# Kernel optimization log

Measured on AMD Instinct MI355X. Metric: run time of the kernel, lower is better.

Reference implementation:

```python
import jax, jax.numpy as jnp
import numpy as np
import math

B, S, H = 512, 100, 1024
A, N = 128, 8
TAU = 1.0


def make_pe(seq_len, hidden):
    # PositionalEncoding buffer: pe[s, 0::2]=sin(pos*div), pe[s,1::2]=cos(pos*div)
    pos = jnp.arange(seq_len, dtype=jnp.float32)[:, None]          # [S,1]
    div = jnp.exp(jnp.arange(0, hidden, 2, dtype=jnp.float32) * (-math.log(10000.0) / hidden))
    pe = jnp.zeros((seq_len, hidden), dtype=jnp.float32)
    pe = pe.at[:, 0::2].set(jnp.sin(pos * div))
    pe = pe.at[:, 1::2].set(jnp.cos(pos * div))
    return pe                                                      # [S,H]


def setup_inputs() -> dict:
    key = jax.random.key(0)
    kx, kq, kk, kg = jax.random.split(key, 4)
    x = jax.random.normal(kx, (B, S, H), dtype=jnp.float32)
    # torch Linear weight layout: [out_features, in_features]
    Wq = jax.random.normal(kq, (A * N, H), dtype=jnp.float32) * (1.0 / math.sqrt(H))
    Wk = jax.random.normal(kk, (A * N, H), dtype=jnp.float32) * (1.0 / math.sqrt(H))
    # pre-sampled standard Gumbel noise (deterministic reference)
    u = jax.random.uniform(kg, (B * N, S), dtype=jnp.float32, minval=1e-6, maxval=1.0 - 1e-6)
    gumbel = -jnp.log(-jnp.log(u))
    return {"x": x, "Wq": Wq, "Wk": Wk, "gumbel": gumbel}


def reference(x, Wq, Wk, gumbel):
    b, s, h = x.shape
    pos_emb = x + make_pe(s, h)[None]                              # [B,S,H]
    Q = (pos_emb @ Wq.T).reshape(b, s, N, A).transpose(0, 2, 1, 3)  # [B,N,S,A]
    K = (pos_emb @ Wk.T).reshape(b, s, N, A).transpose(0, 2, 1, 3)  # [B,N,S,A]
    # original: sum_t (Q . K_t) / sqrt(H) / S  ==  Q . (sum_t K_t) / (sqrt(H)*S)
    Ksum = K.sum(axis=2)                                           # [B,N,A]
    logits = jnp.einsum('bnsa,bna->bns', Q, Ksum) / (math.sqrt(h) * s)
    y = (logits.reshape(b * N, s) + gumbel) / TAU
    soft = jax.nn.softmax(y, axis=-1)
    hard = jax.nn.one_hot(jnp.argmax(y, axis=-1), s, dtype=soft.dtype)
    # straight-through (forward value == hard one-hot)
    alphas = (hard - jax.lax.stop_gradient(soft) + soft).reshape(b, N, s)
    out = jnp.einsum('bns,bsh->bnh', alphas, x)                    # gather selected timesteps
    return out
```

## Files before the change

kernel.cpp:

```cpp
#include <hip/hip_runtime.h>
#include <float.h>
#include <math.h>

#define Bc 512
#define Sc 100
#define Hc 1024
#define Ac 128
#define Nc 8
#define AS_ST 68
#define BS_ST 132

__global__ __launch_bounds__(256) void pe_kernel(float* __restrict__ pe){
  int s = blockIdx.x;
  int t = threadIdx.x;
  const float fac = (float)(-9.210340371976184 / 1024.0);
  for(int i = t; i < Hc/2; i += 256){
    float div = expf((float)(2*i) * fac);
    float a = (float)s * div;
    pe[s*Hc + 2*i]     = sinf(a);
    pe[s*Hc + 2*i + 1] = cosf(a);
  }
}

__global__ __launch_bounds__(256) void pesum_kernel(const float* __restrict__ pe, float* __restrict__ pesum){
  int h = blockIdx.x*256 + threadIdx.x;
  float acc = 0.f;
  for(int s = 0; s < Sc; ++s) acc += pe[s*Hc + h];
  pesum[h] = acc;
}

__global__ __launch_bounds__(256) void xsum_kernel(const float* __restrict__ x, const float* __restrict__ pesum,
                                                   float* __restrict__ xsp){
  int b = blockIdx.x;
  int q = blockIdx.y;
  int t = threadIdx.x;
  const float4* xr = (const float4*)(x + (size_t)b*Sc*Hc);
  float4 acc;
  if(q == 0) acc = ((const float4*)pesum)[t];
  else       acc = make_float4(0.f,0.f,0.f,0.f);
  int s0 = q*25;
  #pragma unroll 5
  for(int s = s0; s < s0+25; ++s){
    float4 v = xr[s*(Hc/4) + t];
    acc.x += v.x; acc.y += v.y; acc.z += v.z; acc.w += v.w;
  }
  ((float4*)(xsp + ((size_t)b*4 + q)*Hc))[t] = acc;
}

__global__ __launch_bounds__(256) void xsred_kernel(const float* __restrict__ xsp, float* __restrict__ xs){
  int b = blockIdx.x, t = threadIdx.x;
  const float4* p = (const float4*)(xsp + (size_t)b*4*Hc);
  float4 a = p[t], b1 = p[256+t], c = p[512+t], d = p[768+t];
  a.x += b1.x + c.x + d.x;
  a.y += b1.y + c.y + d.y;
  a.z += b1.z + c.z + d.z;
  a.w += b1.w + c.w + d.w;
  ((float4*)(xs + (size_t)b*Hc))[t] = a;
}

__global__ __launch_bounds__(256) void ksum_gemm2(const float* __restrict__ xs, const float* __restrict__ Wk,
                                                  float* __restrict__ Ksum4){
  __shared__ float As[32*AS_ST];
  __shared__ float Bs[32*BS_ST];
  const int t = threadIdx.x;
  const int j0 = blockIdx.x*128, b0 = blockIdx.y*64, ks = blockIdx.z;
  const int ty = t>>4, tx = t&15;
  float acc[4][8];
  #pragma unroll
  for(int i = 0; i < 4; ++i)
    #pragma unroll
    for(int j = 0; j < 8; ++j) acc[i][j] = 0.f;

  const int mA = (t>>3) & 63;
  for(int k0 = ks*256; k0 < ks*256 + 256; k0 += 32){
    float4 af[2], bf[4];
    #pragma unroll
    for(int i = 0; i < 2; ++i){
      int id = t + i*256; int m = id>>3, q = id&7;
      af[i] = *(const float4*)(xs + ((size_t)(b0+m)<<10) + k0 + q*4);
    }
    #pragma unroll
    for(int i = 0; i < 4; ++i){
      int id = t + i*256; int r = id>>3, c = id&7;
      bf[i] = *(const float4*)(Wk + ((size_t)(j0+r)<<10) + k0 + c*4);
    }
    __syncthreads();
    #pragma unroll
    for(int i = 0; i < 2; ++i){
      int id = t + i*256; int m = id>>3, q = id&7;
      As[(q*4+0)*AS_ST + m] = af[i].x;
      As[(q*4+1)*AS_ST + m] = af[i].y;
      As[(q*4+2)*AS_ST + m] = af[i].z;
      As[(q*4+3)*AS_ST + m] = af[i].w;
    }
    #pragma unroll
    for(int i = 0; i < 4; ++i){
      int id = t + i*256; int r = id>>3, c = id&7;
      Bs[(c*4+0)*BS_ST + r] = bf[i].x;
      Bs[(c*4+1)*BS_ST + r] = bf[i].y;
      Bs[(c*4+2)*BS_ST + r] = bf[i].z;
      Bs[(c*4+3)*BS_ST + r] = bf[i].w;
    }
    __syncthreads();
    #pragma unroll 8
    for(int kk = 0; kk < 32; ++kk){
      float4 a4 = *(const float4*)&As[kk*AS_ST + ty*4];
      float4 bu = *(const float4*)&Bs[kk*BS_ST + tx*4];
      float4 bv = *(const float4*)&Bs[kk*BS_ST + 64 + tx*4];
      float a[4] = {a4.x, a4.y, a4.z, a4.w};
      float bb[8] = {bu.x,bu.y,bu.z,bu.w, bv.x,bv.y,bv.z,bv.w};
      #pragma unroll
      for(int i = 0; i < 4; ++i)
        #pragma unroll
        for(int j = 0; j < 8; ++j)
          acc[i][j] = fmaf(a[i], bb[j], acc[i][j]);
    }
  }
  (void)mA;
  #pragma unroll
  for(int i = 0; i < 4; ++i){
    float* cp = Ksum4 + (((size_t)ks*Bc + b0 + ty*4 + i)<<10) + j0 + tx*4;
    *(float4*)cp        = make_float4(acc[i][0],acc[i][1],acc[i][2],acc[i][3]);
    *(float4*)(cp + 64) = make_float4(acc[i][4],acc[i][5],acc[i][6],acc[i][7]);
  }
}

__global__ __launch_bounds__(256) void ksred_kernel(const float* __restrict__ Ksum4, float* __restrict__ Ksum){
  int b = blockIdx.x, t = threadIdx.x;
  const float4* p = (const float4*)(Ksum4 + ((size_t)b<<10));
  const size_t sl = (size_t)Bc*Hc/4;
  float4 a = p[t], b1 = p[sl+t], c = p[2*sl+t], d = p[3*sl+t];
  a.x += b1.x + c.x + d.x;
  a.y += b1.y + c.y + d.y;
  a.z += b1.z + c.z + d.z;
  a.w += b1.w + c.w + d.w;
  ((float4*)(Ksum + ((size_t)b<<10)))[t] = a;
}

__global__ __launch_bounds__(256) void v_gemm2(const float* __restrict__ Ksum, const float* __restrict__ Wq,
                                               float* __restrict__ v){
  __shared__ float As[32*AS_ST];
  __shared__ float Bs[32*BS_ST];
  const int t = threadIdx.x;
  const int h0 = blockIdx.x*128, b0 = blockIdx.y*64, n = blockIdx.z;
  const int ty = t>>4, tx = t&15;
  float acc[4][8];
  #pragma unroll
  for(int i = 0; i < 4; ++i)
    #pragma unroll
    for(int j = 0; j < 8; ++j) acc[i][j] = 0.f;

  for(int k0 = 0; k0 < Ac; k0 += 32){
    float4 af[2], bf[4];
    #pragma unroll
    for(int i = 0; i < 2; ++i){
      int id = t + i*256; int m = id>>3, q = id&7;
      af[i] = *(const float4*)(Ksum + ((size_t)(b0+m)<<10) + n*Ac + k0 + q*4);
    }
    #pragma unroll
    for(int i = 0; i < 4; ++i){
      int id = t + i*256; int kk = id>>5, q = id&31;
      bf[i] = *(const float4*)(Wq + ((size_t)(n*Ac + k0 + kk)<<10) + h0 + q*4);
    }
    __syncthreads();
    #pragma unroll
    for(int i = 0; i < 2; ++i){
      int id = t + i*256; int m = id>>3, q = id&7;
      As[(q*4+0)*AS_ST + m] = af[i].x;
      As[(q*4+1)*AS_ST + m] = af[i].y;
      As[(q*4+2)*AS_ST + m] = af[i].z;
      As[(q*4+3)*AS_ST + m] = af[i].w;
    }
    #pragma unroll
    for(int i = 0; i < 4; ++i){
      int id = t + i*256; int kk = id>>5, q = id&31;
      *(float4*)&Bs[kk*BS_ST + q*4] = bf[i];
    }
    __syncthreads();
    #pragma unroll 8
    for(int kk = 0; kk < 32; ++kk){
      float4 a4 = *(const float4*)&As[kk*AS_ST + ty*4];
      float4 bu = *(const float4*)&Bs[kk*BS_ST + tx*4];
      float4 bv = *(const float4*)&Bs[kk*BS_ST + 64 + tx*4];
      float a[4] = {a4.x, a4.y, a4.z, a4.w};
      float bb[8] = {bu.x,bu.y,bu.z,bu.w, bv.x,bv.y,bv.z,bv.w};
      #pragma unroll
      for(int i = 0; i < 4; ++i)
        #pragma unroll
        for(int j = 0; j < 8; ++j)
          acc[i][j] = fmaf(a[i], bb[j], acc[i][j]);
    }
  }
  #pragma unroll
  for(int i = 0; i < 4; ++i){
    float* cp = v + (((size_t)(b0 + ty*4 + i)*Nc + n)<<10) + h0 + tx*4;
    *(float4*)cp        = make_float4(acc[i][0],acc[i][1],acc[i][2],acc[i][3]);
    *(float4*)(cp + 64) = make_float4(acc[i][4],acc[i][5],acc[i][6],acc[i][7]);
  }
}

__global__ __launch_bounds__(1024) void attn_kernel(const float* __restrict__ x, const float* __restrict__ pe,
                                                    const float* __restrict__ v, const float* __restrict__ g,
                                                    float* __restrict__ out){
  __shared__ float4 tile[1600];
  __shared__ float part[8][Nc][104];
  __shared__ int sidx[Nc];
  const int b = blockIdx.x;
  const int t = threadIdx.x;
  const int lane = t & 63;
  const int w  = __builtin_amdgcn_readfirstlane(t >> 6);
  const int kq = w & 7, sh = w >> 3;

  const int r1 = t >> 4, c1 = t & 15;
  const bool has2 = (t < 576);
  const int e2 = t + 1024;
  const int r2 = e2 >> 4, c2 = e2 & 15;

  const float* xb = x + (size_t)b*Sc*Hc;
  const float* vb = v + (size_t)b*Nc*Hc;

  int rw = sh*64 + lane;
  int r  = (rw < Sc) ? rw : (Sc-1);
  const bool valid = (rw < Sc);

  float acc[Nc];
  #pragma unroll
  for(int n = 0; n < Nc; ++n) acc[n] = 0.f;

  float4 xv1 = *(const float4*)(xb + r1*Hc + c1*4);
  float4 pv1 = *(const float4*)(pe + r1*Hc + c1*4);
  float4 xv2 = make_float4(0,0,0,0), pv2 = make_float4(0,0,0,0);
  if(has2){ xv2 = *(const float4*)(xb + r2*Hc + c2*4);
            pv2 = *(const float4*)(pe + r2*Hc + c2*4); }

  for(int kt = 0; kt < 16; ++kt){
    __syncthreads();
    tile[r1*16 + (c1 ^ (r1&7))] = make_float4(xv1.x+pv1.x, xv1.y+pv1.y, xv1.z+pv1.z, xv1.w+pv1.w);
    if(has2)
      tile[r2*16 + (c2 ^ (r2&7))] = make_float4(xv2.x+pv2.x, xv2.y+pv2.y, xv2.z+pv2.z, xv2.w+pv2.w);
    if(kt < 15){
      int ko = (kt+1)*64;
      xv1 = *(const float4*)(xb + r1*Hc + ko + c1*4);
      pv1 = *(const float4*)(pe + r1*Hc + ko + c1*4);
      if(has2){ xv2 = *(const float4*)(xb + r2*Hc + ko + c2*4);
                pv2 = *(const float4*)(pe + r2*Hc + ko + c2*4); }
    }
    __syncthreads();
    #pragma unroll
    for(int j = 0; j < 2; ++j){
      float4 xe = tile[r*16 + ((kq*2 + j) ^ (r&7))];
      const float* vk = vb + kt*64 + kq*8 + j*4;
      #pragma unroll
      for(int n = 0; n < Nc; ++n){
        const float* vn = vk + n*Hc;
        acc[n] = fmaf(xe.x, vn[0], acc[n]);
        acc[n] = fmaf(xe.y, vn[1], acc[n]);
        acc[n] = fmaf(xe.z, vn[2], acc[n]);
        acc[n] = fmaf(xe.w, vn[3], acc[n]);
      }
    }
  }
  if(valid){
    #pragma unroll
    for(int n = 0; n < Nc; ++n) part[kq][n][rw] = acc[n];
  }
  __syncthreads();

  if(w < Nc){
    int n = w, j = lane;
    float best = -FLT_MAX; int bidx = 0;
    #pragma unroll
    for(int i = 0; i < 2; ++i){
      int s2 = j + 64*i;
      if(s2 < Sc){
        float dot = 0.f;
        #pragma unroll
        for(int q = 0; q < 8; ++q) dot += part[q][n][s2];
        float y = dot/3200.0f + g[(size_t)(b*Nc + n)*Sc + s2];
        if(y > best){ best = y; bidx = s2; }
      }
    }
    #pragma unroll
    for(int m = 32; m >= 1; m >>= 1){
      float ob = __shfl_xor(best, m, 64);
      int   oi = __shfl_xor(bidx, m, 64);
      if(ob > best || (ob == best && oi < bidx)){ best = ob; bidx = oi; }
    }
    if(j == 0) sidx[n] = bidx;
  }
  __syncthreads();

  const float4* xb4 = (const float4*)xb;
  float4* ob4 = (float4*)(out + (size_t)b*Nc*Hc);
  #pragma unroll
  for(int i = 0; i < 2; ++i){
    int idx = i*1024 + t;
    int nn = idx >> 8, c = idx & 255;
    ob4[idx] = xb4[sidx[nn]*256 + c];
  }
}

extern "C" void kernel_launch(void* const* d_in, const int* in_sizes, int n_in,
                              void* d_out, int out_size, void* d_ws, size_t ws_size,
                              hipStream_t stream) {
  const float* x  = (const float*)d_in[0];
  const float* Wq = (const float*)d_in[1];
  const float* Wk = (const float*)d_in[2];
  const float* g  = (const float*)d_in[3];
  float* out = (float*)d_out;

  char* ws = (char*)d_ws;
  float* pe    = (float*)(ws);
  float* pesum = (float*)(ws +    409600);
  float* xsp   = (float*)(ws +    413696);
  float* Ksum4 = (float*)(ws +    413696);
  float* xs    = (float*)(ws +   8802304);
  float* Ksum  = (float*)(ws +  10899456);
  float* v     = (float*)(ws +  12996608);

  pe_kernel   <<<100, 256, 0, stream>>>(pe);
  pesum_kernel<<<4,   256, 0, stream>>>(pe, pesum);
  xsum_kernel <<<dim3(512,4), 256, 0, stream>>>(x, pesum, xsp);
  xsred_kernel<<<512, 256, 0, stream>>>(xsp, xs);
  ksum_gemm2  <<<dim3(8,8,4), 256, 0, stream>>>(xs, Wk, Ksum4);
  ksred_kernel<<<512, 256, 0, stream>>>(Ksum4, Ksum);
  v_gemm2     <<<dim3(8,8,8), 256, 0, stream>>>(Ksum, Wq, v);
  attn_kernel <<<512, 1024, 0, stream>>>(x, pe, v, g, out);
}
```

Baseline: 146.4 us.

## Restructure attention logits kernel: wave-per-row with register-resident v and shuffle reductions

```diff
diff --git a/kernel.cpp b/kernel.cpp
--- a/kernel.cpp
+++ b/kernel.cpp
@@ -71,7 +71,6 @@
     #pragma unroll
     for(int j = 0; j < 8; ++j) acc[i][j] = 0.f;
 
-  const int mA = (t>>3) & 63;
   for(int k0 = ks*256; k0 < ks*256 + 256; k0 += 32){
     float4 af[2], bf[4];
     #pragma unroll
@@ -116,7 +115,6 @@
           acc[i][j] = fmaf(a[i], bb[j], acc[i][j]);
     }
   }
-  (void)mA;
   #pragma unroll
   for(int i = 0; i < 4; ++i){
     float* cp = Ksum4 + (((size_t)ks*Bc + b0 + ty*4 + i)<<10) + j0 + tx*4;
@@ -199,70 +197,61 @@
   }
 }
 
-__global__ __launch_bounds__(1024) void attn_kernel(const float* __restrict__ x, const float* __restrict__ pe,
-                                                    const float* __restrict__ v, const float* __restrict__ g,
-                                                    float* __restrict__ out){
-  __shared__ float4 tile[1600];
-  __shared__ float part[8][Nc][104];
+__global__ __launch_bounds__(1024, 8) void attn_kernel(const float* __restrict__ x, const float* __restrict__ pe,
+                                                       const float* __restrict__ v, const float* __restrict__ g,
+                                                       float* __restrict__ out){
+  __shared__ float lg[Sc][9];
   __shared__ int sidx[Nc];
   const int b = blockIdx.x;
   const int t = threadIdx.x;
   const int lane = t & 63;
-  const int w  = __builtin_amdgcn_readfirstlane(t >> 6);
-  const int kq = w & 7, sh = w >> 3;
-
-  const int r1 = t >> 4, c1 = t & 15;
-  const bool has2 = (t < 576);
-  const int e2 = t + 1024;
-  const int r2 = e2 >> 4, c2 = e2 & 15;
-
-  const float* xb = x + (size_t)b*Sc*Hc;
-  const float* vb = v + (size_t)b*Nc*Hc;
-
-  int rw = sh*64 + lane;
-  int r  = (rw < Sc) ? rw : (Sc-1);
-  const bool valid = (rw < Sc);
-
-  float acc[Nc];
-  #pragma unroll
-  for(int n = 0; n < Nc; ++n) acc[n] = 0.f;
-
-  float4 xv1 = *(const float4*)(xb + r1*Hc + c1*4);
-  float4 pv1 = *(const float4*)(pe + r1*Hc + c1*4);
-  float4 xv2 = make_float4(0,0,0,0), pv2 = make_float4(0,0,0,0);
-  if(has2){ xv2 = *(const float4*)(xb + r2*Hc + c2*4);
-            pv2 = *(const float4*)(pe + r2*Hc + c2*4); }
-
-  for(int kt = 0; kt < 16; ++kt){
-    __syncthreads();
-    tile[r1*16 + (c1 ^ (r1&7))] = make_float4(xv1.x+pv1.x, xv1.y+pv1.y, xv1.z+pv1.z, xv1.w+pv1.w);
-    if(has2)
-      tile[r2*16 + (c2 ^ (r2&7))] = make_float4(xv2.x+pv2.x, xv2.y+pv2.y, xv2.z+pv2.z, xv2.w+pv2.w);
-    if(kt < 15){
-      int ko = (kt+1)*64;
-      xv1 = *(const float4*)(xb + r1*Hc + ko + c1*4);
-      pv1 = *(const float4*)(pe + r1*Hc + ko + c1*4);
-      if(has2){ xv2 = *(const float4*)(xb + r2*Hc + ko + c2*4);
-                pv2 = *(const float4*)(pe + r2*Hc + ko + c2*4); }
-    }
-    __syncthreads();
-    #pragma unroll
-    for(int j = 0; j < 2; ++j){
-      float4 xe = tile[r*16 + ((kq*2 + j) ^ (r&7))];
-      const float* vk = vb + kt*64 + kq*8 + j*4;
+  const int w = t >> 6;
+
+  const float4* vb4 = (const float4*)(v + (size_t)b*Nc*Hc);
+  float4 vr[Nc][4];
+  #pragma unroll
+  for(int n = 0; n < Nc; ++n)
+    #pragma unroll
+    for(int i = 0; i < 4; ++i)
+      vr[n][i] = vb4[n*256 + i*64 + lane];
+
+  const float4* xb4 = (const float4*)(x + (size_t)b*Sc*Hc);
+  const float4* pe4 = (const float4*)pe;
+
+  for(int s = w; s < Sc; s += 16){
+    float4 e[4];
+    #pragma unroll
+    for(int i = 0; i < 4; ++i){
+      float4 xv = xb4[s*256 + i*64 + lane];
+      float4 pv = pe4[s*256 + i*64 + lane];
+      e[i] = make_float4(xv.x+pv.x, xv.y+pv.y, xv.z+pv.z, xv.w+pv.w);
+    }
+    float acc[Nc];
+    #pragma unroll
+    for(int n = 0; n < Nc; ++n){
+      float a = 0.f;
       #pragma unroll
-      for(int n = 0; n < Nc; ++n){
-        const float* vn = vk + n*Hc;
-        acc[n] = fmaf(xe.x, vn[0], acc[n]);
-        acc[n] = fmaf(xe.y, vn[1], acc[n]);
-        acc[n] = fmaf(xe.z, vn[2], acc[n]);
-        acc[n] = fmaf(xe.w, vn[3], acc[n]);
+      for(int i = 0; i < 4; ++i){
+        a = fmaf(e[i].x, vr[n][i].x, a);
+        a = fmaf(e[i].y, vr[n][i].y, a);
+        a = fmaf(e[i].z, vr[n][i].z, a);
+        a = fmaf(e[i].w, vr[n][i].w, a);
       }
-    }
-  }
-  if(valid){
-    #pragma unroll
-    for(int n = 0; n < Nc; ++n) part[kq][n][rw] = acc[n];
+      acc[n] = a;
+    }
+    #pragma unroll
+    for(int m = 1; m <= 4; m <<= 1)
+      #pragma unroll
+      for(int n = 0; n < Nc; ++n)
+        acc[n] += __shfl_xor(acc[n], m, 64);
+    float keep = acc[0];
+    #pragma unroll
+    for(int n = 1; n < Nc; ++n)
+      keep = ((lane & 7) == n) ? acc[n] : keep;
+    #pragma unroll
+    for(int m = 8; m <= 32; m <<= 1)
+      keep += __shfl_xor(keep, m, 64);
+    if(lane < Nc) lg[s][lane] = keep;
   }
   __syncthreads();
 
@@ -273,10 +262,7 @@
     for(int i = 0; i < 2; ++i){
       int s2 = j + 64*i;
       if(s2 < Sc){
-        float dot = 0.f;
-        #pragma unroll
-        for(int q = 0; q < 8; ++q) dot += part[q][n][s2];
-        float y = dot/3200.0f + g[(size_t)(b*Nc + n)*Sc + s2];
+        float y = lg[s2][n]/3200.0f + g[(size_t)(b*Nc + n)*Sc + s2];
         if(y > best){ best = y; bidx = s2; }
       }
     }
@@ -290,7 +276,6 @@
   }
   __syncthreads();
 
-  const float4* xb4 = (const float4*)xb;
   float4* ob4 = (float4*)(out + (size_t)b*Nc*Hc);
   #pragma unroll
   for(int i = 0; i < 2; ++i){
```

After: 408.6 us. +179.1%, slower.

## Prefetch next K-chunk into registers in GEMMs and raise ksum split-K to 8

Applied to the files above, without the earlier changes.

```diff
diff --git a/kernel.cpp b/kernel.cpp
--- a/kernel.cpp
+++ b/kernel.cpp
@@ -59,7 +59,7 @@
 }
 
 __global__ __launch_bounds__(256) void ksum_gemm2(const float* __restrict__ xs, const float* __restrict__ Wk,
-                                                  float* __restrict__ Ksum4){
+                                                  float* __restrict__ Ksum8){
   __shared__ float As[32*AS_ST];
   __shared__ float Bs[32*BS_ST];
   const int t = threadIdx.x;
@@ -71,19 +71,20 @@
     #pragma unroll
     for(int j = 0; j < 8; ++j) acc[i][j] = 0.f;
 
-  const int mA = (t>>3) & 63;
-  for(int k0 = ks*256; k0 < ks*256 + 256; k0 += 32){
-    float4 af[2], bf[4];
-    #pragma unroll
-    for(int i = 0; i < 2; ++i){
-      int id = t + i*256; int m = id>>3, q = id&7;
-      af[i] = *(const float4*)(xs + ((size_t)(b0+m)<<10) + k0 + q*4);
-    }
-    #pragma unroll
-    for(int i = 0; i < 4; ++i){
-      int id = t + i*256; int r = id>>3, c = id&7;
-      bf[i] = *(const float4*)(Wk + ((size_t)(j0+r)<<10) + k0 + c*4);
-    }
+  const int kb = ks*128;
+  float4 af[2], bf[4], afn[2], bfn[4];
+  #pragma unroll
+  for(int i = 0; i < 2; ++i){
+    int id = t + i*256; int m = id>>3, q = id&7;
+    af[i] = *(const float4*)(xs + ((size_t)(b0+m)<<10) + kb + q*4);
+  }
+  #pragma unroll
+  for(int i = 0; i < 4; ++i){
+    int id = t + i*256; int r = id>>3, c = id&7;
+    bf[i] = *(const float4*)(Wk + ((size_t)(j0+r)<<10) + kb + c*4);
+  }
+
+  for(int c0 = 0; c0 < 4; ++c0){
     __syncthreads();
     #pragma unroll
     for(int i = 0; i < 2; ++i){
@@ -100,6 +101,19 @@
       Bs[(c*4+1)*BS_ST + r] = bf[i].y;
       Bs[(c*4+2)*BS_ST + r] = bf[i].z;
       Bs[(c*4+3)*BS_ST + r] = bf[i].w;
+    }
+    if(c0 < 3){
+      int k0 = kb + (c0+1)*32;
+      #pragma unroll
+      for(int i = 0; i < 2; ++i){
+        int id = t + i*256; int m = id>>3, q = id&7;
+        afn[i] = *(const float4*)(xs + ((size_t)(b0+m)<<10) + k0 + q*4);
+      }
+      #pragma unroll
+      for(int i = 0; i < 4; ++i){
+        int id = t + i*256; int r = id>>3, c = id&7;
+        bfn[i] = *(const float4*)(Wk + ((size_t)(j0+r)<<10) + k0 + c*4);
+      }
     }
     __syncthreads();
     #pragma unroll 8
@@ -115,25 +129,27 @@
         for(int j = 0; j < 8; ++j)
           acc[i][j] = fmaf(a[i], bb[j], acc[i][j]);
     }
-  }
-  (void)mA;
+    af[0]=afn[0]; af[1]=afn[1];
+    bf[0]=bfn[0]; bf[1]=bfn[1]; bf[2]=bfn[2]; bf[3]=bfn[3];
+  }
   #pragma unroll
   for(int i = 0; i < 4; ++i){
-    float* cp = Ksum4 + (((size_t)ks*Bc + b0 + ty*4 + i)<<10) + j0 + tx*4;
+    float* cp = Ksum8 + (((size_t)ks*Bc + b0 + ty*4 + i)<<10) + j0 + tx*4;
     *(float4*)cp        = make_float4(acc[i][0],acc[i][1],acc[i][2],acc[i][3]);
     *(float4*)(cp + 64) = make_float4(acc[i][4],acc[i][5],acc[i][6],acc[i][7]);
   }
 }
 
-__global__ __launch_bounds__(256) void ksred_kernel(const float* __restrict__ Ksum4, float* __restrict__ Ksum){
+__global__ __launch_bounds__(256) void ksred8_kernel(const float* __restrict__ Ksum8, float* __restrict__ Ksum){
   int b = blockIdx.x, t = threadIdx.x;
-  const float4* p = (const float4*)(Ksum4 + ((size_t)b<<10));
+  const float4* p = (const float4*)(Ksum8 + ((size_t)b<<10));
   const size_t sl = (size_t)Bc*Hc/4;
-  float4 a = p[t], b1 = p[sl+t], c = p[2*sl+t], d = p[3*sl+t];
-  a.x += b1.x + c.x + d.x;
-  a.y += b1.y + c.y + d.y;
-  a.z += b1.z + c.z + d.z;
-  a.w += b1.w + c.w + d.w;
+  float4 a = p[t];
+  #pragma unroll
+  for(int i = 1; i < 8; ++i){
+    float4 q = p[i*sl + t];
+    a.x += q.x; a.y += q.y; a.z += q.z; a.w += q.w;
+  }
   ((float4*)(Ksum + ((size_t)b<<10)))[t] = a;
 }
 
@@ -150,18 +166,19 @@
     #pragma unroll
     for(int j = 0; j < 8; ++j) acc[i][j] = 0.f;
 
-  for(int k0 = 0; k0 < Ac; k0 += 32){
-    float4 af[2], bf[4];
-    #pragma unroll
-    for(int i = 0; i < 2; ++i){
-      int id = t + i*256; int m = id>>3, q = id&7;
-      af[i] = *(const float4*)(Ksum + ((size_t)(b0+m)<<10) + n*Ac + k0 + q*4);
-    }
-    #pragma unroll
-    for(int i = 0; i < 4; ++i){
-      int id = t + i*256; int kk = id>>5, q = id&31;
-      bf[i] = *(const float4*)(Wq + ((size_t)(n*Ac + k0 + kk)<<10) + h0 + q*4);
-    }
+  float4 af[2], bf[4], afn[2], bfn[4];
+  #pragma unroll
+  for(int i = 0; i < 2; ++i){
+    int id = t + i*256; int m = id>>3, q = id&7;
+    af[i] = *(const float4*)(Ksum + ((size_t)(b0+m)<<10) + n*Ac + q*4);
+  }
+  #pragma unroll
+  for(int i = 0; i < 4; ++i){
+    int id = t + i*256; int kk = id>>5, q = id&31;
+    bf[i] = *(const float4*)(Wq + ((size_t)(n*Ac + kk)<<10) + h0 + q*4);
+  }
+
+  for(int c0 = 0; c0 < 4; ++c0){
     __syncthreads();
     #pragma unroll
     for(int i = 0; i < 2; ++i){
@@ -175,6 +192,19 @@
     for(int i = 0; i < 4; ++i){
       int id = t + i*256; int kk = id>>5, q = id&31;
       *(float4*)&Bs[kk*BS_ST + q*4] = bf[i];
+    }
+    if(c0 < 3){
+      int k0 = (c0+1)*32;
+      #pragma unroll
+      for(int i = 0; i < 2; ++i){
+        int id = t + i*256; int m = id>>3, q = id&7;
+        afn[i] = *(const float4*)(Ksum + ((size_t)(b0+m)<<10) + n*Ac + k0 + q*4);
+      }
+      #pragma unroll
+      for(int i = 0; i < 4; ++i){
+        int id = t + i*256; int kk = id>>5, q = id&31;
+        bfn[i] = *(const float4*)(Wq + ((size_t)(n*Ac + k0 + kk)<<10) + h0 + q*4);
+      }
     }
     __syncthreads();
     #pragma unroll 8
@@ -190,6 +220,8 @@
         for(int j = 0; j < 8; ++j)
           acc[i][j] = fmaf(a[i], bb[j], acc[i][j]);
     }
+    af[0]=afn[0]; af[1]=afn[1];
+    bf[0]=bfn[0]; bf[1]=bfn[1]; bf[2]=bfn[2]; bf[3]=bfn[3];
   }
   #pragma unroll
   for(int i = 0; i < 4; ++i){
@@ -313,17 +345,17 @@
   float* pe    = (float*)(ws);
   float* pesum = (float*)(ws +    409600);
   float* xsp   = (float*)(ws +    413696);
-  float* Ksum4 = (float*)(ws +    413696);
   float* xs    = (float*)(ws +   8802304);
-  float* Ksum  = (float*)(ws +  10899456);
-  float* v     = (float*)(ws +  12996608);
-
-  pe_kernel   <<<100, 256, 0, stream>>>(pe);
-  pesum_kernel<<<4,   256, 0, stream>>>(pe, pesum);
-  xsum_kernel <<<dim3(512,4), 256, 0, stream>>>(x, pesum, xsp);
-  xsred_kernel<<<512, 256, 0, stream>>>(xsp, xs);
-  ksum_gemm2  <<<dim3(8,8,4), 256, 0, stream>>>(xs, Wk, Ksum4);
-  ksred_kernel<<<512, 256, 0, stream>>>(Ksum4, Ksum);
-  v_gemm2     <<<dim3(8,8,8), 256, 0, stream>>>(Ksum, Wq, v);
-  attn_kernel <<<512, 1024, 0, stream>>>(x, pe, v, g, out);
-}
+  float* Ksum8 = (float*)(ws +  10899456);
+  float* Ksum  = (float*)(ws +  27676672);
+  float* v     = (float*)(ws +    413696);
+
+  pe_kernel    <<<100, 256, 0, stream>>>(pe);
+  pesum_kernel <<<4,   256, 0, stream>>>(pe, pesum);
+  xsum_kernel  <<<dim3(512,4), 256, 0, stream>>>(x, pesum, xsp);
+  xsred_kernel <<<512, 256, 0, stream>>>(xsp, xs);
+  ksum_gemm2   <<<dim3(8,8,8), 256, 0, stream>>>(xs, Wk, Ksum8);
+  ksred8_kernel<<<512, 256, 0, stream>>>(Ksum8, Ksum);
+  v_gemm2      <<<dim3(8,8,8), 256, 0, stream>>>(Ksum, Wq, v);
+  attn_kernel  <<<512, 1024, 0, stream>>>(x, pe, v, g, out);
+}
```

Result: no change. 146.2 us (-0.1%).
